# Kernel tuning notes

Measured on AMD Instinct MI355X. Metric: run time of the kernel, lower is better.

Reference implementation:

```python
import jax, jax.numpy as jnp
import numpy as np

B, N, T, F_IN = 16, 1024, 12, 1
D_MODEL, D_K, D_V, H, K = 512, 32, 32, 3, 3
C = 32  # nb_chev_filter == nb_time_filter


def _ln(x, g, b, eps=1e-5):
    mu = jnp.mean(x, -1, keepdims=True)
    var = jnp.var(x, -1, keepdims=True)
    return (x - mu) * jax.lax.rsqrt(var + eps) * g + b


def _conv(x, w, b):
    y = jax.lax.conv_general_dilated(x, w, (1, 1), 'VALID',
                                     dimension_numbers=('NCHW', 'OIHW', 'NCHW'))
    return y + b[None, :, None, None]


def setup_inputs() -> dict:
    key = jax.random.key(0)
    ks = iter(jax.random.split(key, 40))
    rn = lambda s, sc=0.02: jax.random.normal(next(ks), s, jnp.float32) * sc
    return dict(
        x=rn((B, N, F_IN, T), 1.0),
        res_att=rn((B, F_IN, H, T, T), 0.1),
        pos_embed_T=rn((T, N)),
        gamma_T=jnp.ones((N,)), beta_T=jnp.zeros((N,)),
        WQ_t=rn((N, D_K * H)), WK_t=rn((N, D_K * H)), WV_t=rn((N, D_V * H)),
        fc_t=rn((H * D_V, N)),
        pre_conv_w=rn((D_MODEL, T, 1, F_IN)), pre_conv_b=rn((D_MODEL,)),
        pos_embed_S=rn((N, D_MODEL)),
        gamma_S=jnp.ones((D_MODEL,)), beta_S=jnp.zeros((D_MODEL,)),
        WQ_s=rn((D_MODEL, D_K * K)), WK_s=rn((D_MODEL, D_K * K)),
        cheb_polys=rn((K, N, N), 0.05),
        adj_pa=(jax.random.uniform(next(ks), (N, N)) < 0.01).astype(jnp.float32),
        cheb_mask=rn((K, N, N)),
        Theta=rn((K, F_IN, C), 0.1),
        gtu3_w=rn((2 * C, C, 1, 3)), gtu3_b=rn((2 * C,)),
        gtu5_w=rn((2 * C, C, 1, 5)), gtu5_b=rn((2 * C,)),
        gtu7_w=rn((2 * C, C, 1, 7)), gtu7_b=rn((2 * C,)),
        res_conv_w=rn((C, F_IN, 1, 1)), res_conv_b=rn((C,)),
        fcmy_w=rn((3 * T - 12, T)), fcmy_b=rn((T,)),
        gamma_f=jnp.ones((C,)), beta_f=jnp.zeros((C,)),
    )


def reference(x, res_att, pos_embed_T, gamma_T, beta_T, WQ_t, WK_t, WV_t, fc_t,
              pre_conv_w, pre_conv_b, pos_embed_S, gamma_S, beta_S, WQ_s, WK_s,
              cheb_polys, adj_pa, cheb_mask, Theta,
              gtu3_w, gtu3_b, gtu5_w, gtu5_b, gtu7_w, gtu7_b,
              res_conv_w, res_conv_b, fcmy_w, fcmy_b, gamma_f, beta_f):
    B_, N_, F_, T_ = x.shape
    # ---- temporal embedding (num_of_features == 1 branch): (B,F,T,N) ----
    TEmx = _ln(jnp.transpose(x, (0, 2, 3, 1)) + pos_embed_T[None, None], gamma_T, beta_T)

    # ---- temporal MHA with residual attention bias ----
    def heads(e, W, d):
        y = e @ W  # (B,F,T,H*d)
        return jnp.transpose(y.reshape(B_, F_, T_, H, d), (0, 1, 3, 2, 4))  # (B,F,H,T,d)
    Q, Kt, V = heads(TEmx, WQ_t, D_K), heads(TEmx, WK_t, D_K), heads(TEmx, WV_t, D_V)
    re_At = jnp.einsum('bfhqd,bfhkd->bfhqk', Q, Kt) / np.sqrt(D_K) + res_att
    attn = jax.nn.softmax(re_At, axis=-1)
    ctx = jnp.einsum('bfhqk,bfhkd->bfhqd', attn, V)
    ctx = jnp.transpose(ctx, (0, 1, 3, 2, 4)).reshape(B_, F_, T_, H * D_V)
    one_n, zero_n = jnp.ones((N_,), x.dtype), jnp.zeros((N_,), x.dtype)
    TATout = _ln(ctx @ fc_t + TEmx, one_n, zero_n)  # fresh LayerNorm(d_model) -> gamma=1, beta=0

    # ---- pre_conv: Conv2d(T, d_model, kernel=(1,F)) on (B,T,N,F); take last col ----
    x_TAt = jnp.einsum('btnf,dtf->bnd', jnp.transpose(TATout, (0, 2, 3, 1)),
                       pre_conv_w[:, :, 0, :]) + pre_conv_b  # (B,N,d_model)

    # ---- spatial embedding + spatial attention scores (no softmax) ----
    SEmx = _ln(x_TAt + pos_embed_S[None], gamma_S, beta_S)  # dropout = identity (eval)
    Qs = jnp.transpose((SEmx @ WQ_s).reshape(B_, N_, K, D_K), (0, 2, 1, 3))
    Ks = jnp.transpose((SEmx @ WK_s).reshape(B_, N_, K, D_K), (0, 2, 1, 3))
    STAt = jnp.einsum('bknd,bkmd->bknm', Qs, Ks) / np.sqrt(D_K)  # (B,K,N,N)

    # ---- Chebyshev graph conv weighted by spatial attention ----
    satt = jax.nn.softmax(STAt + (adj_pa[None] * cheb_mask)[None], axis=2)
    Tka = cheb_polys[None] * satt  # (B,K,N,N)
    rhs = jnp.einsum('bkmn,bmft->bknft', Tka, x)  # T_k_with_at^T @ x over all t
    spatial_gcn = jax.nn.relu(jnp.einsum('bknft,kfo->bnot', rhs, Theta))  # (B,N,C,T)

    # ---- gated temporal convs (GTU) ----
    X = jnp.transpose(spatial_gcn, (0, 2, 1, 3))  # (B,C,N,T)
    def gtu(w, b):
        y = _conv(X, w, b)
        return jnp.tanh(y[:, :C]) * jax.nn.sigmoid(y[:, C:])
    time_conv = jnp.concatenate([gtu(gtu3_w, gtu3_b), gtu(gtu5_w, gtu5_b),
                                 gtu(gtu7_w, gtu7_b)], axis=-1)  # (B,C,N,3T-12)
    time_conv = time_conv @ fcmy_w + fcmy_b  # (B,C,N,T)
    tco = jax.nn.relu(time_conv)  # num_of_features == 1 branch

    # ---- residual 1x1 conv + final LayerNorm over channel dim ----
    x_res = _conv(jnp.transpose(x, (0, 2, 1, 3)), res_conv_w, res_conv_b)  # (B,C,N,T)
    out = _ln(jnp.transpose(jax.nn.relu(x_res + tco), (0, 3, 2, 1)), gamma_f, beta_f)
    out = jnp.transpose(out, (0, 2, 3, 1))  # (B,N,C,T)
    return out, re_At
```

## Files before the change

### kernel.cpp

```cpp
#include <hip/hip_runtime.h>
#include <hip/hip_bf16.h>
#include <math.h>

#define B_ 16
#define N_ 1024
#define T_ 12
#define DM_ 512
#define H_ 3
#define K_ 3
#define C_ 32
#define RSQRT_DK 0.17677669529663687f

typedef __attribute__((ext_vector_type(8))) short bf16x8;
typedef __attribute__((ext_vector_type(4))) float f32x4;

__device__ __forceinline__ ushort f2bf(float f) {
  uint u = __float_as_uint(f);
  return (ushort)((u + 0x7FFF + ((u >> 16) & 1)) >> 16);
}
__device__ __forceinline__ float bf2f(ushort h) {
  return __uint_as_float(((uint)h) << 16);
}

__global__ void k1_temporal_ln(const float* __restrict__ x, const float* __restrict__ posT,
                               const float* __restrict__ gT, const float* __restrict__ bT,
                               float* __restrict__ TEmx) {
  int row = blockIdx.x;
  int b = row / T_, t = row - b * T_;
  __shared__ float red[256], red2[256];
  float v[4]; float s = 0.f, s2 = 0.f;
  for (int i = 0; i < 4; ++i) {
    int n = threadIdx.x + (i << 8);
    float val = x[(b * N_ + n) * T_ + t] + posT[t * N_ + n];
    v[i] = val; s += val; s2 += val * val;
  }
  red[threadIdx.x] = s; red2[threadIdx.x] = s2;
  __syncthreads();
  for (int off = 128; off > 0; off >>= 1) {
    if (threadIdx.x < off) { red[threadIdx.x] += red[threadIdx.x + off]; red2[threadIdx.x] += red2[threadIdx.x + off]; }
    __syncthreads();
  }
  float mu = red[0] * (1.f / N_);
  float rs = rsqrtf(red2[0] * (1.f / N_) - mu * mu + 1e-5f);
  for (int i = 0; i < 4; ++i) {
    int n = threadIdx.x + (i << 8);
    TEmx[row * N_ + n] = (v[i] - mu) * rs * gT[n] + bT[n];
  }
}

__global__ __launch_bounds__(256) void k2_qkv(const float* __restrict__ TEmx,
                       const float* __restrict__ WQ, const float* __restrict__ WK,
                       const float* __restrict__ WV, float* __restrict__ part) {
  int kc = blockIdx.x, row = blockIdx.y;
  __shared__ float e[256];
  int tid = threadIdx.x;
  e[tid] = TEmx[row * N_ + kc * 256 + tid];
  __syncthreads();
  for (int col = tid; col < 288; col += 256) {
    int which = col / 96, j = col - which * 96;
    const float* W = (which == 0) ? WQ : ((which == 1) ? WK : WV);
    const float* Wp = W + (size_t)(kc * 256) * 96 + j;
    float acc = 0.f;
    #pragma unroll 8
    for (int n = 0; n < 256; ++n) acc += e[n] * Wp[n * 96];
    part[(row * 4 + kc) * 288 + col] = acc;
  }
}

__global__ __launch_bounds__(256) void k3a_attn(const float* __restrict__ part, const float* __restrict__ res_att,
                         float* __restrict__ reAt_out, float* __restrict__ ctx) {
  int bh = blockIdx.x;
  int b = bh / 3, h = bh - b * 3;
  __shared__ float q_l[3 * T_ * 32];
  __shared__ float s_l[T_ * T_];
  int tid = threadIdx.x;
  for (int i = tid; i < 1152; i += 256) {
    int sec = i / 384, r = i - sec * 384, t = r >> 5, d = r & 31;
    int col = sec * 96 + h * 32 + d;
    const float* pr = &part[(size_t)((b * T_ + t) * 4) * 288 + col];
    q_l[i] = pr[0] + pr[288] + pr[576] + pr[864];
  }
  __syncthreads();
  if (tid < 144) {
    int qi = tid / 12, ki = tid - qi * 12;
    float acc = 0.f;
    #pragma unroll
    for (int d = 0; d < 32; ++d)
      acc += q_l[qi * 32 + d] * q_l[384 + ki * 32 + d];
    float sv = acc * RSQRT_DK + res_att[(size_t)bh * 144 + tid];
    s_l[tid] = sv;
    reAt_out[(size_t)bh * 144 + tid] = sv;
  }
  __syncthreads();
  if (tid < 12) {
    float mx = -1e30f;
    for (int ki = 0; ki < 12; ++ki) mx = fmaxf(mx, s_l[tid * 12 + ki]);
    float sum = 0.f;
    for (int ki = 0; ki < 12; ++ki) { float p = __expf(s_l[tid * 12 + ki] - mx); s_l[tid * 12 + ki] = p; sum += p; }
    float inv = 1.f / sum;
    for (int ki = 0; ki < 12; ++ki) s_l[tid * 12 + ki] *= inv;
  }
  __syncthreads();
  for (int i = tid; i < 384; i += 256) {
    int qi = i >> 5, d = i & 31;
    float acc = 0.f;
    for (int ki = 0; ki < 12; ++ki)
      acc += s_l[qi * 12 + ki] * q_l[768 + ki * 32 + d];
    ctx[(size_t)(b * T_ + qi) * 96 + h * 32 + d] = acc;
  }
}

__global__ __launch_bounds__(1024) void k3b_tat(const float* __restrict__ ctx,
                        const float* __restrict__ fc_t,
                        const float* __restrict__ TEmx, float* __restrict__ TAT) {
  int row = blockIdx.x;
  __shared__ float c_l[96];
  __shared__ float red[16], red2[16];
  int tid = threadIdx.x;
  if (tid < 96) c_l[tid] = ctx[row * 96 + tid];
  __syncthreads();
  float acc = TEmx[row * N_ + tid];
  #pragma unroll 12
  for (int j = 0; j < 96; ++j) acc = fmaf(c_l[j], fc_t[j * N_ + tid], acc);
  float s = acc, s2 = acc * acc;
  #pragma unroll
  for (int off = 32; off > 0; off >>= 1) {
    s  += __shfl_xor(s, off);
    s2 += __shfl_xor(s2, off);
  }
  int w = tid >> 6;
  if ((tid & 63) == 0) { red[w] = s; red2[w] = s2; }
  __syncthreads();
  float ts = 0.f, ts2 = 0.f;
  #pragma unroll
  for (int i = 0; i < 16; ++i) { ts += red[i]; ts2 += red2[i]; }
  float mu = ts * (1.f / N_);
  float rs = rsqrtf(ts2 * (1.f / N_) - mu * mu + 1e-5f);
  TAT[row * N_ + tid] = (acc - mu) * rs;
}

__global__ __launch_bounds__(256) void k4_preconv_ln(const float* __restrict__ TAT, const float* __restrict__ pcw,
                              const float* __restrict__ pcb, const float* __restrict__ posS,
                              const float* __restrict__ gS, const float* __restrict__ bS,
                              float* __restrict__ SEmx) {
  int wid = blockIdx.x * 4 + (threadIdx.x >> 6);
  int b = wid >> 10, n = wid & 1023;
  int lane = threadIdx.x & 63;
  float tc[12];
  #pragma unroll
  for (int t = 0; t < 12; ++t) tc[t] = TAT[(b * T_ + t) * N_ + n];
  float v[8]; float s = 0.f, s2 = 0.f;
  #pragma unroll
  for (int i = 0; i < 8; ++i) {
    int d = lane + (i << 6);
    const float4* pw = (const float4*)&pcw[d * 12];
    float4 w0 = pw[0], w1 = pw[1], w2 = pw[2];
    float acc = pcb[d];
    acc += tc[0] * w0.x + tc[1] * w0.y + tc[2] * w0.z + tc[3] * w0.w;
    acc += tc[4] * w1.x + tc[5] * w1.y + tc[6] * w1.z + tc[7] * w1.w;
    acc += tc[8] * w2.x + tc[9] * w2.y + tc[10] * w2.z + tc[11] * w2.w;
    acc += posS[(size_t)n * DM_ + d];
    v[i] = acc; s += acc; s2 += acc * acc;
  }
  #pragma unroll
  for (int off = 1; off < 64; off <<= 1) {
    s  += __shfl_xor(s, off);
    s2 += __shfl_xor(s2, off);
  }
  float mu = s * (1.f / DM_);
  float rs = rsqrtf(s2 * (1.f / DM_) - mu * mu + 1e-5f);
  #pragma unroll
  for (int i = 0; i < 8; ++i) {
    int d = lane + (i << 6);
    SEmx[(size_t)wid * DM_ + d] = (v[i] - mu) * rs * gS[d] + bS[d];
  }
}

__global__ void k5_pre(const float* __restrict__ WQs, const float* __restrict__ WKs,
                       ushort* __restrict__ wpre) {
  int idx = blockIdx.x * 256 + threadIdx.x;
  int k = idx / 192, col = idx - k * 192;
  float v = (col < 96) ? WQs[k * 96 + col] : WKs[k * 96 + (col - 96)];
  wpre[col * 512 + k] = f2bf(v);
}

__global__ void k8_pre(const float* __restrict__ w3, const float* __restrict__ w5,
                       const float* __restrict__ w7, ushort* __restrict__ wg) {
  int idx = blockIdx.x * 256 + threadIdx.x;
  if (idx < 6144) {
    int dt = idx / 2048, rem = idx - dt * 2048, co = rem >> 5, ic = rem & 31;
    wg[idx] = f2bf(w3[(co * 32 + ic) * 3 + dt]);
  } else if (idx < 16384) {
    int ds = idx - 6144;
    int dt = ds / 2048, rem = ds - dt * 2048, co = rem >> 5, ic = rem & 31;
    wg[idx] = f2bf(w5[(co * 32 + ic) * 5 + dt]);
  } else if (idx < 30720) {
    int ds = idx - 16384;
    int dt = ds / 2048, rem = ds - dt * 2048, co = rem >> 5, ic = rem & 31;
    wg[idx] = f2bf(w7[(co * 32 + ic) * 7 + dt]);
  }
}

__global__ __launch_bounds__(256) void k5_qks(const float* __restrict__ SEmx,
                                              const ushort* __restrict__ wpre,
                                              __hip_bfloat16* __restrict__ Qs,
                                              __hip_bfloat16* __restrict__ Ks) {
  int b = blockIdx.y, n0 = blockIdx.x * 32;
  __shared__ __align__(16) ushort SE_h[32 * 520];
  int tid = threadIdx.x;
  for (int idx = tid; idx < 4096; idx += 256) {
    int r = idx >> 7, cq = idx & 127;
    float4 v = *(const float4*)&SEmx[((size_t)((b << 10) + n0 + r)) * DM_ + cq * 4];
    uint lo = (uint)f2bf(v.x) | ((uint)f2bf(v.y) << 16);
    uint hi = (uint)f2bf(v.z) | ((uint)f2bf(v.w) << 16);
    *(uint2*)&SE_h[r * 520 + cq * 4] = make_uint2(lo, hi);
  }
  __syncthreads();

  int w = tid >> 6, lane = tid & 63, quad = lane >> 4, c16 = lane & 15;
  f32x4 acc[3][2];
  #pragma unroll
  for (int mi = 0; mi < 3; ++mi)
    #pragma unroll
    for (int nt = 0; nt < 2; ++nt) acc[mi][nt] = (f32x4){0.f, 0.f, 0.f, 0.f};

  for (int ks = 0; ks < 16; ++ks) {
    bf16x8 Bf0 = *(const bf16x8*)&SE_h[(0 * 16 + c16) * 520 + ks * 32 + quad * 8];
    bf16x8 Bf1 = *(const bf16x8*)&SE_h[(1 * 16 + c16) * 520 + ks * 32 + quad * 8];
    #pragma unroll
    for (int mi = 0; mi < 3; ++mi) {
      int m = (w * 3 + mi) * 16 + c16;
      bf16x8 Af = *(const bf16x8*)&wpre[m * 512 + ks * 32 + quad * 8];
      acc[mi][0] = __builtin_amdgcn_mfma_f32_16x16x32_bf16(Af, Bf0, acc[mi][0], 0, 0, 0);
      acc[mi][1] = __builtin_amdgcn_mfma_f32_16x16x32_bf16(Af, Bf1, acc[mi][1], 0, 0, 0);
    }
  }
  #pragma unroll
  for (int mi = 0; mi < 3; ++mi) {
    int mb = (w * 3 + mi) * 16;
    #pragma unroll
    for (int nt = 0; nt < 2; ++nt) {
      int node = n0 + nt * 16 + c16;
      #pragma unroll
      for (int r = 0; r < 4; ++r) {
        int m = mb + quad * 4 + r;
        int j = (m < 96) ? m : m - 96;
        int kk = j >> 5, dd = j & 31;
        __hip_bfloat16* o = (m < 96) ? Qs : Ks;
        o[(((b * K_ + kk) * N_) + node) * 32 + dd] = __float2bfloat16(acc[mi][nt][r]);
      }
    }
  }
}

__global__ void k6_pre(const float* __restrict__ adj, const float* __restrict__ mask,
                       const float* __restrict__ cheb, uint* __restrict__ pk) {
  int idx = (blockIdx.x * 256 + threadIdx.x) * 4;
  int mn = idx & (N_ * N_ - 1);
  float4 a = *(const float4*)&adj[mn];
  float4 m = *(const float4*)&mask[idx];
  float4 c = *(const float4*)&cheb[idx];
  uint4 o;
  o.x = (uint)f2bf(a.x * m.x) | ((uint)f2bf(c.x) << 16);
  o.y = (uint)f2bf(a.y * m.y) | ((uint)f2bf(c.y) << 16);
  o.z = (uint)f2bf(a.z * m.z) | ((uint)f2bf(c.z) << 16);
  o.w = (uint)f2bf(a.w * m.w) | ((uint)f2bf(c.w) << 16);
  *(uint4*)&pk[idx] = o;
}

__global__ __launch_bounds__(256) void k6_spatial(
    const __hip_bfloat16* __restrict__ Qs, const __hip_bfloat16* __restrict__ Ks,
    const uint* __restrict__ pk, const float* __restrict__ x,
    float* __restrict__ rhs) {
  const int d  = blockIdx.x;
  const int q_ = d >> 3;
  const int b  = q_ & 15;
  const int g  = ((q_ >> 4) << 3) | (d & 7);
  const int k  = g >> 5;
  const int n0 = (g & 31) << 5;
  const ushort* Qb = (const ushort*)(Qs + (size_t)((b * K_ + k) * N_) * 32);
  const ushort* Kb = (const ushort*)(Ks + (size_t)((b * K_ + k) * N_) * 32);
  const uint* pkk = pk + (size_t)k * (N_ * N_);
  const float* xb = x + b * N_ * T_;

  __shared__ float well[4][32];
  __shared__ float wacc[4][32][12];

  const int tid  = threadIdx.x;
  const int w    = tid >> 6, lane = tid & 63;
  const int quad = lane >> 4, c16 = lane & 15;

  bf16x8 bfr0 = *(const bf16x8*)(Kb + (size_t)(n0 + c16) * 32 + quad * 8);
  bf16x8 bfr1 = *(const bf16x8*)(Kb + (size_t)(n0 + 16 + c16) * 32 + quad * 8);

  float el0 = 0.f, el1 = 0.f;
  float acc0[12], acc1[12];
  #pragma unroll
  for (int t = 0; t < 12; ++t) { acc0[t] = 0.f; acc1[t] = 0.f; }

  for (int s = 0; s < 16; ++s) {
    const int m0 = s * 64 + w * 16;
    bf16x8 af = *(const bf16x8*)(Qb + (size_t)(m0 + c16) * 32 + quad * 8);
    f32x4 z = {0.f, 0.f, 0.f, 0.f};
    f32x4 sc0 = __builtin_amdgcn_mfma_f32_16x16x32_bf16(af, bfr0, z, 0, 0, 0);
    f32x4 sc1 = __builtin_amdgcn_mfma_f32_16x16x32_bf16(af, bfr1, z, 0, 0, 0);

    const int mrow = m0 + quad * 4;
    float p0[4], p1[4];
    #pragma unroll
    for (int r = 0; r < 4; ++r) {
      uint p2 = pkk[(size_t)(mrow + r) * N_ + n0 + c16];
      uint q2 = pkk[(size_t)(mrow + r) * N_ + n0 + 16 + c16];
      float sv0 = sc0[r] * RSQRT_DK + __uint_as_float(p2 << 16);
      float sv1 = sc1[r] * RSQRT_DK + __uint_as_float(q2 << 16);
      p0[r] = __expf(sv0); el0 += p0[r];
      p0[r] *= __uint_as_float(p2 & 0xFFFF0000u);
      p1[r] = __expf(sv1); el1 += p1[r];
      p1[r] *= __uint_as_float(q2 & 0xFFFF0000u);
    }
    #pragma unroll
    for (int r = 0; r < 4; ++r) {
      const float4* xr = (const float4*)(xb + (size_t)(mrow + r) * 12);
      float4 xA = xr[0], xB = xr[1], xC = xr[2];
      float xv[12] = {xA.x, xA.y, xA.z, xA.w, xB.x, xB.y, xB.z, xB.w,
                      xC.x, xC.y, xC.z, xC.w};
      float px0 = p0[r], px1 = p1[r];
      #pragma unroll
      for (int t = 0; t < 12; ++t) {
        acc0[t] = fmaf(px0, xv[t], acc0[t]);
        acc1[t] = fmaf(px1, xv[t], acc1[t]);
      }
    }
  }

  #pragma unroll
  for (int off = 16; off <= 32; off <<= 1) {
    el0 += __shfl_xor(el0, off);
    el1 += __shfl_xor(el1, off);
    #pragma unroll
    for (int t = 0; t < 12; ++t) {
      acc0[t] += __shfl_xor(acc0[t], off);
      acc1[t] += __shfl_xor(acc1[t], off);
    }
  }
  if (quad == 0) {
    well[w][c16] = el0;
    #pragma unroll
    for (int t = 0; t < 12; ++t) wacc[w][c16][t] = acc0[t];
  } else if (quad == 1) {
    well[w][16 + c16] = el1;
    #pragma unroll
    for (int t = 0; t < 12; ++t) wacc[w][16 + c16][t] = acc1[t];
  }
  __syncthreads();
  if (tid < 384) {
    int n = tid / 12, t = tid - n * 12;
    float den = well[0][n] + well[1][n] + well[2][n] + well[3][n];
    float num = wacc[0][n][t] + wacc[1][n][t] + wacc[2][n][t] + wacc[3][n][t];
    rhs[((size_t)(b * K_ + k) * N_ + n0 + n) * 12 + t] = num / den;
  }
}

template<int KS, int JV, int JB, int WOFF>
__device__ __forceinline__ void conv_mfma_g(const ushort* X_th, const ushort* __restrict__ wg,
                                            ushort* tc_h, const float* bias0,
                                            int mp, int ntg, int quad, int c16) {
  f32x4 accA[3], accB[3];
  #pragma unroll
  for (int i = 0; i < 3; ++i) { accA[i] = (f32x4){0.f,0.f,0.f,0.f}; accB[i] = (f32x4){0.f,0.f,0.f,0.f}; }
  #pragma unroll
  for (int dt = 0; dt < KS; ++dt) {
    bf16x8 A0 = *(const bf16x8*)&wg[WOFF + (dt * 64 + mp * 16 + c16) * 32 + quad * 8];
    bf16x8 A1 = *(const bf16x8*)&wg[WOFF + (dt * 64 + (mp + 2) * 16 + c16) * 32 + quad * 8];
    #pragma unroll
    for (int i = 0; i < 3; ++i) {
      int nt = ntg * 3 + i;
      int j = nt >> 1, sh = nt & 1;
      bf16x8 Bf = *(const bf16x8*)&X_th[(sh * 16 + c16) * 584 + (j + dt) * 32 + quad * 8];
      accA[i] = __builtin_amdgcn_mfma_f32_16x16x32_bf16(A0, Bf, accA[i], 0, 0, 0);
      accB[i] = __builtin_amdgcn_mfma_f32_16x16x32_bf16(A1, Bf, accB[i], 0, 0, 0);
    }
  }
  int sxq = ((quad & 1) << 5) ^ ((quad & 2) << 1);
  #pragma unroll
  for (int i = 0; i < 3; ++i) {
    int nt = ntg * 3 + i, j = nt >> 1, sh = nt & 1;
    if (j < JV) {
      int s = sh * 16 + c16;
      int sx = ((s & 15) << 1) ^ sxq;
      #pragma unroll
      for (int r = 0; r < 4; ++r) {
        int cc = mp * 16 + quad * 4 + r;
        float a = accA[i][r] + bias0[cc];
        float g = accB[i][r] + bias0[cc + 32];
        float e2a = __expf(2.f * a);
        float th = 1.f - 2.f / (e2a + 1.f);
        float sg = 1.f / (1.f + __expf(-g));
        tc_h[((s * 32 + cc) * 32 + (JB + j)) ^ sx] = f2bf(th * sg);
      }
    }
  }
}

__global__ __launch_bounds__(1024) void k8_fused(
                       const float* __restrict__ rhs, const float* __restrict__ Theta,
                       const float* __restrict__ x, const float* __restrict__ rw,
                       const float* __restrict__ rb,
                       const ushort* __restrict__ wg,
                       const float* __restrict__ b3, const float* __restrict__ b5,
                       const float* __restrict__ b7,
                       const float* __restrict__ fw, const float* __restrict__ fb,
                       const float* __restrict__ gf, const float* __restrict__ bf,
                       float* __restrict__ out) {
  int bn0 = blockIdx.x * 32;
  int b = bn0 >> 10, n0 = bn0 & 1023;

  __shared__ __align__(16) char uR[50176];
  ushort* X_th = (ushort*)uR;
  float*  v_l  = (float*)uR;
  __shared__ __align__(16) ushort tc_h[1024 * 32];
  __shared__ float rhs_l[32 * 36];
  __shared__ float Th_l[96];
  __shared__ float xr_l[32 * 12];
  __shared__ float fw_l[288];
  __shared__ float fb_l[12];
  __shared__ float bias_l[3][64];
  __shared__ float rw_l[32], rb_l[32], gf_l[32], bf_l[32];
  __shared__ float stm[384], str[384];

  int tid = threadIdx.x;
  int w = tid >> 6, lane = tid & 63, quad = lane >> 4, c16 = lane & 15;
  int mp = w & 1, ntg = w >> 1;
  int c = (tid >> 3) & 31;
  int site = (tid & 7) | ((tid >> 8) << 3);

  for (int idx = tid; idx < 1152; idx += 1024) {
    int s = idx / 36, r = idx - s * 36, k = r / 12, t = r - k * 12;
    rhs_l[idx] = rhs[((size_t)(b * 3 + k) * N_ + n0 + s) * 12 + t];
  }
  if (tid < 384) xr_l[tid] = x[(size_t)(b * N_ + n0) * 12 + tid];
  if (tid < 96) Th_l[tid] = Theta[tid];
  if (tid < 288) fw_l[tid] = fw[tid];
  if (tid < 12) fb_l[tid] = fb[tid];
  if (tid < 64) { bias_l[0][tid] = b3[tid]; bias_l[1][tid] = b5[tid]; bias_l[2][tid] = b7[tid]; }
  if (tid >= 64 && tid < 96)  rw_l[tid - 64] = rw[tid - 64];
  if (tid >= 96 && tid < 128) rb_l[tid - 96] = rb[tid - 96];
  if (tid >= 128 && tid < 160) gf_l[tid - 128] = gf[tid - 128];
  if (tid >= 160 && tid < 192) bf_l[tid - 160] = bf[tid - 160];
  __syncthreads();

  {
    float th0 = Th_l[c], th1 = Th_l[32 + c], th2 = Th_l[64 + c];
    const float* rs_ = &rhs_l[site * 36];
    ushort* xo = &X_th[site * 584 + c];
    #pragma unroll
    for (int t = 0; t < 12; ++t) {
      float a = rs_[t] * th0 + rs_[12 + t] * th1 + rs_[24 + t] * th2;
      xo[t * 32] = f2bf(fmaxf(a, 0.f));
    }
  }
  for (int idx = tid; idx < 32 * 6 * 32; idx += 1024) {
    int s = idx / 192, r2 = idx - s * 192, tt = r2 >> 5, ic = r2 & 31;
    X_th[s * 584 + (12 + tt) * 32 + ic] = 0;
  }
  __syncthreads();

  conv_mfma_g<3, 10, 0,      0>(X_th, wg, tc_h, &bias_l[0][0], mp, ntg, quad, c16);
  conv_mfma_g<5, 8, 10,   6144>(X_th, wg, tc_h, &bias_l[1][0], mp, ntg, quad, c16);
  conv_mfma_g<7, 6, 18,  16384>(X_th, wg, tc_h, &bias_l[2][0], mp, ntg, quad, c16);
  __syncthreads();

  float tcv[24];
  {
    int rb2 = (site * 32 + c) * 32;
    int sxr = ((site & 15) << 1) ^ ((c & 4) << 3) ^ ((c & 8) >> 1);
    #pragma unroll
    for (int j = 0; j < 24; ++j)
      tcv[j] = __uint_as_float(((uint)tc_h[(rb2 + j) ^ sxr]) << 16);
  }
  float o[12];
  #pragma unroll
  for (int t = 0; t < 12; ++t) o[t] = fb_l[t];
  #pragma unroll
  for (int j = 0; j < 24; ++j) {
    const float4* fp = (const float4*)&fw_l[j * 12];
    float4 f0 = fp[0], f1 = fp[1], f2 = fp[2];
    float fr[12] = {f0.x, f0.y, f0.z, f0.w, f1.x, f1.y, f1.z, f1.w, f2.x, f2.y, f2.z, f2.w};
    #pragma unroll
    for (int t = 0; t < 12; ++t) o[t] = fmaf(tcv[j], fr[t], o[t]);
  }

  float v[12];
  {
    float rwc = rw_l[c], rbc = rb_l[c];
    const float* xs = &xr_l[site * 12];
    float* vo = &v_l[site * 391 + c * 12];
    #pragma unroll
    for (int t = 0; t < 12; ++t) {
      float xres = xs[t] * rwc + rbc;
      v[t] = fmaxf(xres + fmaxf(o[t], 0.f), 0.f);
      vo[t] = v[t];
    }
  }
  __syncthreads();
  if (tid < 384) {
    int s = tid / 12, t = tid - s * 12;
    float sm = 0.f, s2 = 0.f;
    #pragma unroll 8
    for (int cc = 0; cc < 32; ++cc) {
      float u = v_l[s * 391 + cc * 12 + t];
      sm += u; s2 += u * u;
    }
    float m = sm * (1.f / 32.f);
    stm[tid] = m;
    str[tid] = rsqrtf(s2 * (1.f / 32.f) - m * m + 1e-5f);
  }
  __syncthreads();
  {
    float gfc = gf_l[c], bfc = bf_l[c];
    const float* sm_ = &stm[site * 12];
    const float* sr_ = &str[site * 12];
    float q[12];
    #pragma unroll
    for (int t = 0; t < 12; ++t) q[t] = (v[t] - sm_[t]) * sr_[t] * gfc + bfc;
    float* op = &out[(size_t)(bn0 + site) * 384 + c * 12];
    ((float4*)op)[0] = make_float4(q[0], q[1], q[2], q[3]);
    ((float4*)op)[1] = make_float4(q[4], q[5], q[6], q[7]);
    ((float4*)op)[2] = make_float4(q[8], q[9], q[10], q[11]);
  }
}

extern "C" void kernel_launch(void* const* d_in, const int* in_sizes, int n_in,
                              void* d_out, int out_size, void* d_ws, size_t ws_size,
                              hipStream_t stream) {
  const float* x       = (const float*)d_in[0];
  const float* res_att = (const float*)d_in[1];
  const float* posT    = (const float*)d_in[2];
  const float* gT      = (const float*)d_in[3];
  const float* bT      = (const float*)d_in[4];
  const float* WQt     = (const float*)d_in[5];
  const float* WKt     = (const float*)d_in[6];
  const float* WVt     = (const float*)d_in[7];
  const float* fct     = (const float*)d_in[8];
  const float* pcw     = (const float*)d_in[9];
  const float* pcb     = (const float*)d_in[10];
  const float* posS    = (const float*)d_in[11];
  const float* gS      = (const float*)d_in[12];
  const float* bS      = (const float*)d_in[13];
  const float* WQs     = (const float*)d_in[14];
  const float* WKs     = (const float*)d_in[15];
  const float* cheb    = (const float*)d_in[16];
  const float* adj     = (const float*)d_in[17];
  const float* mask    = (const float*)d_in[18];
  const float* Theta   = (const float*)d_in[19];
  const float* w3      = (const float*)d_in[20];
  const float* b3      = (const float*)d_in[21];
  const float* w5      = (const float*)d_in[22];
  const float* b5      = (const float*)d_in[23];
  const float* w7      = (const float*)d_in[24];
  const float* b7      = (const float*)d_in[25];
  const float* rw      = (const float*)d_in[26];
  const float* rb      = (const float*)d_in[27];
  const float* fw      = (const float*)d_in[28];
  const float* fb      = (const float*)d_in[29];
  const float* gf      = (const float*)d_in[30];
  const float* bf      = (const float*)d_in[31];

  float* ws = (float*)d_ws;
  float* TEmx = ws;
  float* qkv  = TEmx + 196608;
  float* ctx  = qkv + 55296;
  float* TAT  = ctx + 18432;
  float* SEmx = TAT + 196608;
  float* Qsf  = SEmx + 8388608;
  float* Ksf  = Qsf + 1572864;
  float* rhs  = Ksf + 1572864;
  ushort* wpre = (ushort*)(rhs + 589824);
  ushort* wg   = (ushort*)qkv;
  float* part = SEmx;

  __hip_bfloat16* Qh = (__hip_bfloat16*)Qsf;
  __hip_bfloat16* Kh = (__hip_bfloat16*)Ksf;
  uint* pk = (uint*)SEmx;

  float* out  = (float*)d_out;
  float* reAt = out + 6291456;

  k5_pre<<<(DM_ * 192) / 256, 256, 0, stream>>>(WQs, WKs, wpre);
  k8_pre<<<120, 256, 0, stream>>>(w3, w5, w7, wg);
  k1_temporal_ln<<<B_ * T_, 256, 0, stream>>>(x, posT, gT, bT, TEmx);
  k2_qkv<<<dim3(4, B_ * T_), 256, 0, stream>>>(TEmx, WQt, WKt, WVt, part);
  k3a_attn<<<B_ * H_, 256, 0, stream>>>(part, res_att, reAt, ctx);
  k3b_tat<<<B_ * T_, 1024, 0, stream>>>(ctx, fct, TEmx, TAT);
  k4_preconv_ln<<<B_ * N_ / 4, 256, 0, stream>>>(TAT, pcw, pcb, posS, gS, bS, SEmx);
  k5_qks<<<dim3(N_ / 32, B_), 256, 0, stream>>>(SEmx, wpre, Qh, Kh);
  k6_pre<<<(K_ * N_ * N_) / 1024, 256, 0, stream>>>(adj, mask, cheb, pk);
  k6_spatial<<<B_ * K_ * (N_ / 32), 256, 0, stream>>>(Qh, Kh, pk, x, rhs);
  k8_fused<<<B_ * N_ / 32, 1024, 0, stream>>>(rhs, Theta, x, rw, rb,
                                              wg, b3, b5, b7, fw, fb, gf, bf, out);
}
```

Measured before the change: 315.5 us.

## Fuse pre-conv LayerNorm into QK projection and merge prepack kernels

Computes the spatial pre-conv and LayerNorm directly into shared memory inside the Q/K projection kernel, so the fp32 SEmx intermediate (16x1024x512 floats) is no longer written to and read back from global memory. The three weight and mask prepack kernels are merged into one launch that runs at the start of the pipeline, which removes launches and lets the cheb/mask packing overlap earlier work. The pk buffer is moved to an offset inside the SEmx region to avoid clashing with other uses. Each QK block now recomputes the LayerNorm for its 32 nodes with fewer waves in flight than the old standalone kernel.

New measurement: 302.4 us. 4.2% less time.

```diff
diff --git a/kernel.cpp b/kernel.cpp
--- a/kernel.cpp
+++ b/kernel.cpp
@@ -139,85 +139,96 @@
   TAT[row * N_ + tid] = (acc - mu) * rs;
 }
 
-__global__ __launch_bounds__(256) void k4_preconv_ln(const float* __restrict__ TAT, const float* __restrict__ pcw,
-                              const float* __restrict__ pcb, const float* __restrict__ posS,
-                              const float* __restrict__ gS, const float* __restrict__ bS,
-                              float* __restrict__ SEmx) {
-  int wid = blockIdx.x * 4 + (threadIdx.x >> 6);
-  int b = wid >> 10, n = wid & 1023;
-  int lane = threadIdx.x & 63;
-  float tc[12];
-  #pragma unroll
-  for (int t = 0; t < 12; ++t) tc[t] = TAT[(b * T_ + t) * N_ + n];
-  float v[8]; float s = 0.f, s2 = 0.f;
-  #pragma unroll
-  for (int i = 0; i < 8; ++i) {
-    int d = lane + (i << 6);
-    const float4* pw = (const float4*)&pcw[d * 12];
-    float4 w0 = pw[0], w1 = pw[1], w2 = pw[2];
-    float acc = pcb[d];
-    acc += tc[0] * w0.x + tc[1] * w0.y + tc[2] * w0.z + tc[3] * w0.w;
-    acc += tc[4] * w1.x + tc[5] * w1.y + tc[6] * w1.z + tc[7] * w1.w;
-    acc += tc[8] * w2.x + tc[9] * w2.y + tc[10] * w2.z + tc[11] * w2.w;
-    acc += posS[(size_t)n * DM_ + d];
-    v[i] = acc; s += acc; s2 += acc * acc;
-  }
-  #pragma unroll
-  for (int off = 1; off < 64; off <<= 1) {
-    s  += __shfl_xor(s, off);
-    s2 += __shfl_xor(s2, off);
-  }
-  float mu = s * (1.f / DM_);
-  float rs = rsqrtf(s2 * (1.f / DM_) - mu * mu + 1e-5f);
-  #pragma unroll
-  for (int i = 0; i < 8; ++i) {
-    int d = lane + (i << 6);
-    SEmx[(size_t)wid * DM_ + d] = (v[i] - mu) * rs * gS[d] + bS[d];
-  }
-}
-
-__global__ void k5_pre(const float* __restrict__ WQs, const float* __restrict__ WKs,
-                       ushort* __restrict__ wpre) {
-  int idx = blockIdx.x * 256 + threadIdx.x;
-  int k = idx / 192, col = idx - k * 192;
-  float v = (col < 96) ? WQs[k * 96 + col] : WKs[k * 96 + (col - 96)];
-  wpre[col * 512 + k] = f2bf(v);
-}
-
-__global__ void k8_pre(const float* __restrict__ w3, const float* __restrict__ w5,
-                       const float* __restrict__ w7, ushort* __restrict__ wg) {
-  int idx = blockIdx.x * 256 + threadIdx.x;
-  if (idx < 6144) {
-    int dt = idx / 2048, rem = idx - dt * 2048, co = rem >> 5, ic = rem & 31;
-    wg[idx] = f2bf(w3[(co * 32 + ic) * 3 + dt]);
-  } else if (idx < 16384) {
-    int ds = idx - 6144;
-    int dt = ds / 2048, rem = ds - dt * 2048, co = rem >> 5, ic = rem & 31;
-    wg[idx] = f2bf(w5[(co * 32 + ic) * 5 + dt]);
-  } else if (idx < 30720) {
-    int ds = idx - 16384;
-    int dt = ds / 2048, rem = ds - dt * 2048, co = rem >> 5, ic = rem & 31;
-    wg[idx] = f2bf(w7[(co * 32 + ic) * 7 + dt]);
-  }
-}
-
-__global__ __launch_bounds__(256) void k5_qks(const float* __restrict__ SEmx,
+__global__ __launch_bounds__(256) void k_prepack(
+    const float* __restrict__ adj, const float* __restrict__ mask,
+    const float* __restrict__ cheb, uint* __restrict__ pk,
+    const float* __restrict__ WQs, const float* __restrict__ WKs,
+    ushort* __restrict__ wpre,
+    const float* __restrict__ w3, const float* __restrict__ w5,
+    const float* __restrict__ w7, ushort* __restrict__ wg) {
+  int bid = blockIdx.x, tid = threadIdx.x;
+  if (bid < 3072) {
+    int idx = (bid * 256 + tid) * 4;
+    int mn = idx & (N_ * N_ - 1);
+    float4 a = *(const float4*)&adj[mn];
+    float4 m = *(const float4*)&mask[idx];
+    float4 c = *(const float4*)&cheb[idx];
+    uint4 o;
+    o.x = (uint)f2bf(a.x * m.x) | ((uint)f2bf(c.x) << 16);
+    o.y = (uint)f2bf(a.y * m.y) | ((uint)f2bf(c.y) << 16);
+    o.z = (uint)f2bf(a.z * m.z) | ((uint)f2bf(c.z) << 16);
+    o.w = (uint)f2bf(a.w * m.w) | ((uint)f2bf(c.w) << 16);
+    *(uint4*)&pk[idx] = o;
+  } else if (bid < 3456) {
+    int idx = (bid - 3072) * 256 + tid;
+    int k = idx / 192, col = idx - k * 192;
+    float v = (col < 96) ? WQs[k * 96 + col] : WKs[k * 96 + (col - 96)];
+    wpre[col * 512 + k] = f2bf(v);
+  } else {
+    int idx = (bid - 3456) * 256 + tid;
+    if (idx < 6144) {
+      int dt = idx / 2048, rem = idx - dt * 2048, co = rem >> 5, ic = rem & 31;
+      wg[idx] = f2bf(w3[(co * 32 + ic) * 3 + dt]);
+    } else if (idx < 16384) {
+      int ds = idx - 6144;
+      int dt = ds / 2048, rem = ds - dt * 2048, co = rem >> 5, ic = rem & 31;
+      wg[idx] = f2bf(w5[(co * 32 + ic) * 5 + dt]);
+    } else if (idx < 30720) {
+      int ds = idx - 16384;
+      int dt = ds / 2048, rem = ds - dt * 2048, co = rem >> 5, ic = rem & 31;
+      wg[idx] = f2bf(w7[(co * 32 + ic) * 7 + dt]);
+    }
+  }
+}
+
+__global__ __launch_bounds__(256) void k5_qks(const float* __restrict__ TAT,
+                                              const float* __restrict__ pcw,
+                                              const float* __restrict__ pcb,
+                                              const float* __restrict__ posS,
+                                              const float* __restrict__ gS,
+                                              const float* __restrict__ bS,
                                               const ushort* __restrict__ wpre,
                                               __hip_bfloat16* __restrict__ Qs,
                                               __hip_bfloat16* __restrict__ Ks) {
   int b = blockIdx.y, n0 = blockIdx.x * 32;
   __shared__ __align__(16) ushort SE_h[32 * 520];
   int tid = threadIdx.x;
-  for (int idx = tid; idx < 4096; idx += 256) {
-    int r = idx >> 7, cq = idx & 127;
-    float4 v = *(const float4*)&SEmx[((size_t)((b << 10) + n0 + r)) * DM_ + cq * 4];
-    uint lo = (uint)f2bf(v.x) | ((uint)f2bf(v.y) << 16);
-    uint hi = (uint)f2bf(v.z) | ((uint)f2bf(v.w) << 16);
-    *(uint2*)&SE_h[r * 520 + cq * 4] = make_uint2(lo, hi);
-  }
-  __syncthreads();
-
-  int w = tid >> 6, lane = tid & 63, quad = lane >> 4, c16 = lane & 15;
+  int w = tid >> 6, lane = tid & 63, quad = (lane >> 4), c16 = lane & 15;
+
+  for (int j = 0; j < 8; ++j) {
+    int r = w * 8 + j;
+    int n = n0 + r;
+    float tc[12];
+    #pragma unroll
+    for (int t = 0; t < 12; ++t) tc[t] = TAT[(size_t)(b * T_ + t) * N_ + n];
+    float vv[8]; float s = 0.f, s2 = 0.f;
+    #pragma unroll
+    for (int i = 0; i < 8; ++i) {
+      int dd = lane + (i << 6);
+      const float4* pw = (const float4*)&pcw[dd * 12];
+      float4 w0 = pw[0], w1 = pw[1], w2 = pw[2];
+      float acc = pcb[dd];
+      acc += tc[0] * w0.x + tc[1] * w0.y + tc[2] * w0.z + tc[3] * w0.w;
+      acc += tc[4] * w1.x + tc[5] * w1.y + tc[6] * w1.z + tc[7] * w1.w;
+      acc += tc[8] * w2.x + tc[9] * w2.y + tc[10] * w2.z + tc[11] * w2.w;
+      acc += posS[(size_t)n * DM_ + dd];
+      vv[i] = acc; s += acc; s2 += acc * acc;
+    }
+    #pragma unroll
+    for (int off = 1; off < 64; off <<= 1) {
+      s  += __shfl_xor(s, off);
+      s2 += __shfl_xor(s2, off);
+    }
+    float mu = s * (1.f / DM_);
+    float rs = rsqrtf(s2 * (1.f / DM_) - mu * mu + 1e-5f);
+    #pragma unroll
+    for (int i = 0; i < 8; ++i) {
+      int dd = lane + (i << 6);
+      SE_h[r * 520 + dd] = f2bf((vv[i] - mu) * rs * gS[dd] + bS[dd]);
+    }
+  }
+  __syncthreads();
+
   f32x4 acc[3][2];
   #pragma unroll
   for (int mi = 0; mi < 3; ++mi)
@@ -251,21 +262,6 @@
       }
     }
   }
-}
-
-__global__ void k6_pre(const float* __restrict__ adj, const float* __restrict__ mask,
-                       const float* __restrict__ cheb, uint* __restrict__ pk) {
-  int idx = (blockIdx.x * 256 + threadIdx.x) * 4;
-  int mn = idx & (N_ * N_ - 1);
-  float4 a = *(const float4*)&adj[mn];
-  float4 m = *(const float4*)&mask[idx];
-  float4 c = *(const float4*)&cheb[idx];
-  uint4 o;
-  o.x = (uint)f2bf(a.x * m.x) | ((uint)f2bf(c.x) << 16);
-  o.y = (uint)f2bf(a.y * m.y) | ((uint)f2bf(c.y) << 16);
-  o.z = (uint)f2bf(a.z * m.z) | ((uint)f2bf(c.z) << 16);
-  o.w = (uint)f2bf(a.w * m.w) | ((uint)f2bf(c.w) << 16);
-  *(uint4*)&pk[idx] = o;
 }
 
 __global__ __launch_bounds__(256) void k6_spatial(
@@ -581,20 +577,18 @@
 
   __hip_bfloat16* Qh = (__hip_bfloat16*)Qsf;
   __hip_bfloat16* Kh = (__hip_bfloat16*)Ksf;
-  uint* pk = (uint*)SEmx;
+  uint* pk = (uint*)(SEmx + 1048576);
 
   float* out  = (float*)d_out;
   float* reAt = out + 6291456;
 
-  k5_pre<<<(DM_ * 192) / 256, 256, 0, stream>>>(WQs, WKs, wpre);
-  k8_pre<<<120, 256, 0, stream>>>(w3, w5, w7, wg);
+  k_prepack<<<3576, 256, 0, stream>>>(adj, mask, cheb, pk, WQs, WKs, wpre,
+                                      w3, w5, w7, wg);
   k1_temporal_ln<<<B_ * T_, 256, 0, stream>>>(x, posT, gT, bT, TEmx);
   k2_qkv<<<dim3(4, B_ * T_), 256, 0, stream>>>(TEmx, WQt, WKt, WVt, part);
   k3a_attn<<<B_ * H_, 256, 0, stream>>>(part, res_att, reAt, ctx);
   k3b_tat<<<B_ * T_, 1024, 0, stream>>>(ctx, fct, TEmx, TAT);
-  k4_preconv_ln<<<B_ * N_ / 4, 256, 0, stream>>>(TAT, pcw, pcb, posS, gS, bS, SEmx);
-  k5_qks<<<dim3(N_ / 32, B_), 256, 0, stream>>>(SEmx, wpre, Qh, Kh);
-  k6_pre<<<(K_ * N_ * N_) / 1024, 256, 0, stream>>>(adj, mask, cheb, pk);
+  k5_qks<<<dim3(N_ / 32, B_), 256, 0, stream>>>(TAT, pcw, pcb, posS, gS, bS, wpre, Qh, Kh);
   k6_spatial<<<B_ * K_ * (N_ / 32), 256, 0, stream>>>(Qh, Kh, pk, x, rhs);
   k8_fused<<<B_ * N_ / 32, 1024, 0, stream>>>(rhs, Theta, x, rw, rb,
                                               wg, b3, b5, b7, fw, fb, gf, bf, out);
```
